# Kernel tuning notes

Measured on AMD Instinct MI355X. Metric: run time of the kernel, lower is better.

## Reference

```python
import jax, jax.numpy as jnp
import numpy as np
from jax import lax

PHI_WIDTH = 1.0  # default width of the Phi play-operator

def _phi(x):
    # Phi(x) = max(0, x) + min(0, x + width)
    return jnp.maximum(0.0, x) + jnp.minimum(0.0, x + PHI_WIDTH)

def setup_inputs() -> dict:
    key = jax.random.key(0)
    T = 16_777_216  # number of recurrence steps; input has T+1 entries
    inputs = jax.random.normal(key, (T + 1,), dtype=jnp.float32)
    kernel = jnp.float32(1.0)  # scalar trainable weight (self.weight = 1.0)
    return {"inputs": inputs, "kernel": kernel}

def reference(inputs, kernel):
    # p0 is the initial state; remaining entries are the driving signal
    p0 = inputs[0]
    x = inputs[1:] * kernel  # [T]

    def step(y_prev, xt):
        y = _phi(xt - y_prev) + y_prev
        return y, y

    _, ys = lax.scan(step, p0, x)  # ys: [T]
    return jnp.concatenate([p0[None], ys])  # [T+1], matches tf.convert_to_tensor(outputs)
```

## Files before the change

### kernel.cpp

```cpp
#include <hip/hip_runtime.h>
#include <math.h>


#define TPB 256
#define EPT 4
#define EPB (TPB * EPT)
#define NW  (TPB / 64)
#define HCH TPB

struct Pair { float a, b; };

__device__ __forceinline__ float med3f(float x, float lo, float hi) {
    return __builtin_amdgcn_fmed3f(x, lo, hi);
}
__device__ __forceinline__ Pair compose(Pair l, Pair r) {
    Pair o; o.a = med3f(l.a, r.a, r.b); o.b = med3f(l.b, r.a, r.b); return o;
}
__device__ __forceinline__ Pair ident() {
    Pair p; p.a = -INFINITY; p.b = INFINITY; return p;
}

__global__ __launch_bounds__(TPB)
void k_scan(const float* __restrict__ in, const float* __restrict__ kptr,
            float* __restrict__ out, int n) {
    const int tid  = threadIdx.x, lane = tid & 63, wid = tid >> 6;
    const int vid  = blockIdx.x;
    const int tile0 = vid * EPB;
    const int base  = tile0 + tid * EPT;
    const float k   = kptr[0];
    const bool blockFull = (tile0 + EPB <= n);

    __shared__ Pair wS[NW];
    __shared__ Pair wC[NW];

    float ta[EPT], tb[EPT];
    {
        float a = -INFINITY, b = INFINITY;
        if (blockFull) {
            float4 f = *reinterpret_cast<const float4*>(in + base);
            float xv[4] = {f.x, f.y, f.z, f.w};
            #pragma unroll
            for (int j = 0; j < 4; ++j) {
                float lo = xv[j] * k, hi = lo + 1.0f;
                if (j == 0 && base == 0) { lo = xv[0]; hi = xv[0]; }
                a = med3f(a, lo, hi);
                b = med3f(b, lo, hi);
                ta[j] = a; tb[j] = b;
            }
        } else {
            #pragma unroll
            for (int j = 0; j < EPT; ++j) {
                if (base + j < n) {
                    float x = in[base + j];
                    float lo = x * k, hi = lo + 1.0f;
                    if (j == 0 && base == 0) { lo = x; hi = x; }
                    a = med3f(a, lo, hi);
                    b = med3f(b, lo, hi);
                }
                ta[j] = a; tb[j] = b;
            }
        }
    }

    Pair w; w.a = ta[EPT - 1]; w.b = tb[EPT - 1];
    #pragma unroll
    for (int off = 1; off < 64; off <<= 1) {
        Pair u; u.a = __shfl_up(w.a, off); u.b = __shfl_up(w.b, off);
        if (lane >= off) w = compose(u, w);
    }
    if (lane == 63) wS[wid] = w;
    __syncthreads();
    Pair wpre = ident();
    #pragma unroll
    for (int i = 0; i < NW; ++i) if (i < wid) wpre = compose(wpre, wS[i]);
    Pair up; up.a = __shfl_up(w.a, 1); up.b = __shfl_up(w.b, 1);
    Pair ex = (lane == 0) ? wpre : compose(wpre, up);

    Pair S = ident();
    int chunkEnd = tile0;
    while (chunkEnd > 0) {
        const int chunkStart = chunkEnd - HCH;
        const int e = chunkStart + tid;
        Pair wnd;
        {
            float x  = in[e];
            float lo = x * k, hi = lo + 1.0f;
            if (e == 0) { lo = x; hi = x; }
            wnd.a = lo; wnd.b = hi;
        }
        #pragma unroll
        for (int off = 1; off < 64; off <<= 1) {
            Pair u; u.a = __shfl_down(wnd.a, off); u.b = __shfl_down(wnd.b, off);
            Pair c = compose(wnd, u);
            if (lane + off < 64) wnd = c;
        }
        if (lane == 0) wC[wid] = wnd;
        __syncthreads();
        Pair cagg = wC[0];
        #pragma unroll
        for (int i = 1; i < NW; ++i) cagg = compose(cagg, wC[i]);
        __syncthreads();
        S = compose(cagg, S);
        if (S.a == S.b) break;
        chunkEnd = chunkStart;
    }
    const float ysrc = med3f(0.0f, S.a, S.b);

    const float ytin = med3f(ysrc, ex.a, ex.b);
    if (blockFull) {
        float4 o;
        o.x = med3f(ytin, ta[0], tb[0]);
        o.y = med3f(ytin, ta[1], tb[1]);
        o.z = med3f(ytin, ta[2], tb[2]);
        o.w = med3f(ytin, ta[3], tb[3]);
        *reinterpret_cast<float4*>(out + base) = o;
    } else {
        #pragma unroll
        for (int j = 0; j < EPT; ++j)
            if (base + j < n) out[base + j] = med3f(ytin, ta[j], tb[j]);
    }
}

extern "C" void kernel_launch(void* const* d_in, const int* in_sizes, int n_in,
                              void* d_out, int out_size, void* d_ws, size_t ws_size,
                              hipStream_t stream) {
    const float* in   = (const float*)d_in[0];
    const float* kptr = (const float*)d_in[1];
    float* out = (float*)d_out;
    const int n  = in_sizes[0];
    const int nb = (n + EPB - 1) / EPB;

    k_scan<<<nb, TPB, 0, stream>>>(in, kptr, out, n);
}
```

Baseline: 32.07 us.

## Process four coalesced groups per block to amortize look-back prefix search

```diff
diff --git a/kernel.cpp b/kernel.cpp
--- a/kernel.cpp
+++ b/kernel.cpp
@@ -3,10 +3,11 @@
 
 
 #define TPB 256
-#define EPT 4
-#define EPB (TPB * EPT)
+#define GPB 4
+#define GSZ (TPB * 4)
+#define EPB (GPB * GSZ)
 #define NW  (TPB / 64)
-#define HCH TPB
+#define HCH 256
 
 struct Pair { float a, b; };
 
@@ -26,64 +27,61 @@
     const int tid  = threadIdx.x, lane = tid & 63, wid = tid >> 6;
     const int vid  = blockIdx.x;
     const int tile0 = vid * EPB;
-    const int base  = tile0 + tid * EPT;
     const float k   = kptr[0];
     const bool blockFull = (tile0 + EPB <= n);
 
-    __shared__ Pair wS[NW];
+    __shared__ Pair wS[GPB][NW];
     __shared__ Pair wC[NW];
 
-    float ta[EPT], tb[EPT];
-    {
+    float hx = 0.0f;
+    if (tile0 > 0) hx = in[tile0 - HCH + tid];
+
+    float ta[GPB][4], tb[GPB][4];
+    Pair  upv[GPB];
+    #pragma unroll
+    for (int v = 0; v < GPB; ++v) {
+        const int b4 = tile0 + v * GSZ + 4 * tid;
+        float xv[4];
+        if (blockFull) {
+            float4 f = reinterpret_cast<const float4*>(in + tile0 + v * GSZ)[tid];
+            xv[0] = f.x; xv[1] = f.y; xv[2] = f.z; xv[3] = f.w;
+        } else {
+            #pragma unroll
+            for (int j = 0; j < 4; ++j)
+                xv[j] = (b4 + j < n) ? in[b4 + j] : 0.0f;
+        }
         float a = -INFINITY, b = INFINITY;
-        if (blockFull) {
-            float4 f = *reinterpret_cast<const float4*>(in + base);
-            float xv[4] = {f.x, f.y, f.z, f.w};
-            #pragma unroll
-            for (int j = 0; j < 4; ++j) {
+        #pragma unroll
+        for (int j = 0; j < 4; ++j) {
+            if (blockFull || b4 + j < n) {
                 float lo = xv[j] * k, hi = lo + 1.0f;
-                if (j == 0 && base == 0) { lo = xv[0]; hi = xv[0]; }
+                if (j == 0 && b4 == 0) { lo = xv[0]; hi = xv[0]; }
                 a = med3f(a, lo, hi);
                 b = med3f(b, lo, hi);
-                ta[j] = a; tb[j] = b;
             }
-        } else {
-            #pragma unroll
-            for (int j = 0; j < EPT; ++j) {
-                if (base + j < n) {
-                    float x = in[base + j];
-                    float lo = x * k, hi = lo + 1.0f;
-                    if (j == 0 && base == 0) { lo = x; hi = x; }
-                    a = med3f(a, lo, hi);
-                    b = med3f(b, lo, hi);
-                }
-                ta[j] = a; tb[j] = b;
-            }
+            ta[v][j] = a; tb[v][j] = b;
         }
+        Pair w; w.a = a; w.b = b;
+        #pragma unroll
+        for (int off = 1; off < 64; off <<= 1) {
+            Pair u; u.a = __shfl_up(w.a, off); u.b = __shfl_up(w.b, off);
+            if (lane >= off) w = compose(u, w);
+        }
+        upv[v].a = __shfl_up(w.a, 1); upv[v].b = __shfl_up(w.b, 1);
+        if (lane == 63) wS[v][wid] = w;
     }
-
-    Pair w; w.a = ta[EPT - 1]; w.b = tb[EPT - 1];
-    #pragma unroll
-    for (int off = 1; off < 64; off <<= 1) {
-        Pair u; u.a = __shfl_up(w.a, off); u.b = __shfl_up(w.b, off);
-        if (lane >= off) w = compose(u, w);
-    }
-    if (lane == 63) wS[wid] = w;
     __syncthreads();
-    Pair wpre = ident();
-    #pragma unroll
-    for (int i = 0; i < NW; ++i) if (i < wid) wpre = compose(wpre, wS[i]);
-    Pair up; up.a = __shfl_up(w.a, 1); up.b = __shfl_up(w.b, 1);
-    Pair ex = (lane == 0) ? wpre : compose(wpre, up);
 
     Pair S = ident();
     int chunkEnd = tile0;
+    bool first = true;
     while (chunkEnd > 0) {
         const int chunkStart = chunkEnd - HCH;
         const int e = chunkStart + tid;
+        float x = first ? hx : in[e];
+        first = false;
         Pair wnd;
         {
-            float x  = in[e];
             float lo = x * k, hi = lo + 1.0f;
             if (e == 0) { lo = x; hi = x; }
             wnd.a = lo; wnd.b = hi;
@@ -104,20 +102,33 @@
         if (S.a == S.b) break;
         chunkEnd = chunkStart;
     }
-    const float ysrc = med3f(0.0f, S.a, S.b);
+    float y = med3f(0.0f, S.a, S.b);
 
-    const float ytin = med3f(ysrc, ex.a, ex.b);
-    if (blockFull) {
-        float4 o;
-        o.x = med3f(ytin, ta[0], tb[0]);
-        o.y = med3f(ytin, ta[1], tb[1]);
-        o.z = med3f(ytin, ta[2], tb[2]);
-        o.w = med3f(ytin, ta[3], tb[3]);
-        *reinterpret_cast<float4*>(out + base) = o;
-    } else {
+    #pragma unroll
+    for (int v = 0; v < GPB; ++v) {
+        Pair wpre = ident();
         #pragma unroll
-        for (int j = 0; j < EPT; ++j)
-            if (base + j < n) out[base + j] = med3f(ytin, ta[j], tb[j]);
+        for (int i = 0; i < NW; ++i) if (i < wid) wpre = compose(wpre, wS[v][i]);
+        Pair ex = (lane == 0) ? wpre : compose(wpre, upv[v]);
+        const float ytin = med3f(y, ex.a, ex.b);
+        Pair G = wS[v][0];
+        #pragma unroll
+        for (int i = 1; i < NW; ++i) G = compose(G, wS[v][i]);
+        y = med3f(y, G.a, G.b);
+
+        const int b4 = tile0 + v * GSZ + 4 * tid;
+        if (blockFull) {
+            float4 o;
+            o.x = med3f(ytin, ta[v][0], tb[v][0]);
+            o.y = med3f(ytin, ta[v][1], tb[v][1]);
+            o.z = med3f(ytin, ta[v][2], tb[v][2]);
+            o.w = med3f(ytin, ta[v][3], tb[v][3]);
+            reinterpret_cast<float4*>(out + tile0 + v * GSZ)[tid] = o;
+        } else {
+            #pragma unroll
+            for (int j = 0; j < 4; ++j)
+                if (b4 + j < n) out[b4 + j] = med3f(ytin, ta[v][j], tb[v][j]);
+        }
     }
 }
 
```

After: 27.95 us. 12.8% less time.
